# Kernel optimization log

Hardware: AMD Instinct MI355X
Metric: run time of the kernel (lower is better)

## Reference

```python
import jax, jax.numpy as jnp
import numpy as np

HEADS = 8
KS = 7
PAD = 3


def grouped_conv1x1(x, w):
    # x: (B, Cin, H, W), w: (heads, Cout/h, Cin/h) -> (B, Cout, H, W)
    B, Cin, H, W = x.shape
    g, co, ci = w.shape
    xg = x.reshape(B, g, ci, H, W)
    out = jnp.einsum('bgchw,goc->bgohw', xg, w)
    return out.reshape(B, g * co, H, W)


def unfold2d(p, k):
    # p: (B, C, Hp, Wp) -> (B, C, H, W, k, k) sliding windows, stride 1
    B, C, Hp, Wp = p.shape
    H, W = Hp - k + 1, Wp - k + 1
    rows = [jnp.stack([p[:, :, i:i + H, j:j + W] for j in range(k)], axis=-1)
            for i in range(k)]
    return jnp.stack(rows, axis=-2)  # (B,C,H,W,k,k)


def setup_inputs() -> dict:
    key = jax.random.key(0)
    ks = jax.random.split(key, 7)
    B, Cin, H, W = 8, 64, 64, 64
    Cout = 64
    g = HEADS
    return {
        'x': jax.random.normal(ks[0], (B, Cin, H, W), jnp.float32),
        'r': jax.random.normal(ks[1], (1,), jnp.float32),
        'w_q': jax.random.normal(ks[2], (g, Cout // g, Cin // g), jnp.float32) * 0.2,
        'w_k': jax.random.normal(ks[3], (g, Cout // g, Cin // g), jnp.float32) * 0.2,
        'w_v': jax.random.normal(ks[4], (g, Cout // g, Cin // g), jnp.float32) * 0.2,
        'rel_h': jax.random.normal(ks[5], (Cout // 2, KS), jnp.float32),
        'rel_w': jax.random.normal(ks[6], (Cout // 2, KS), jnp.float32),
    }


def reference(x, r, w_q, w_k, w_v, rel_h, rel_w):
    B, Cin, H, W = x.shape
    g = HEADS
    Cout = w_q.shape[0] * w_q.shape[1]
    dh = Cout // g

    padded = jnp.pad(x, ((0, 0), (0, 0), (PAD, PAD), (PAD, PAD)))
    q = grouped_conv1x1(x, w_q)            # (B, Cout, H, W)
    k = grouped_conv1x1(padded, w_k)       # (B, Cout, H+2p, W+2p)
    v = grouped_conv1x1(padded, w_v)

    k = unfold2d(k, KS)                    # (B, Cout, H, W, KS, KS)
    v = unfold2d(v, KS)

    # learnable relative positional encoding: split channels in half,
    # add rel_h along window-height, rel_w along window-width
    half = Cout // 2
    k_h = k[:, :half] + rel_h[None, :, None, None, :, None]
    k_w = k[:, half:] + rel_w[None, :, None, None, None, :]
    k = jnp.concatenate([k_h, k_w], axis=1)

    K2 = KS * KS
    k = k.reshape(B, g, dh, H, W, K2)
    v = v.reshape(B, g, dh, H, W, K2)
    q = q.reshape(B, g, dh, H, W, 1)

    scale = np.sqrt(g / Cout).astype(np.float32)
    logits = (q * k).sum(axis=2, keepdims=True) * scale   # (B,g,1,H,W,K2)
    attn = jax.nn.softmax(logits, axis=-1)
    out = (attn * v).sum(axis=-1)                          # (B,g,dh,H,W)
    return out.reshape(B, Cout, H, W)
```

## Files before the change

kernel.cpp:

```cpp
#include <hip/hip_runtime.h>
#include <math.h>

#define NG  8
#define DH  8
#define NCP 4
#define KS  7
#define PAD 3
#define TH  16
#define TW  32
#define OW  2
#define TPH 22
#define RSTW 40
#define PLW  (TPH * RSTW)
#define CH  64
#define HH  64
#define WW  64

typedef __fp16 h2v __attribute__((ext_vector_type(2)));
typedef __fp16 h4v __attribute__((ext_vector_type(4)));

#if __has_builtin(__builtin_amdgcn_exp2f)
#define EXP2(x) __builtin_amdgcn_exp2f(x)
#else
#define EXP2(x) exp2f(x)
#endif

__device__ __forceinline__ int imin(int a, int b) { return a < b ? a : b; }
__device__ __forceinline__ int imax(int a, int b) { return a > b ? a : b; }

__global__ __launch_bounds__(256, 2)
void saconv_kernel(const float* __restrict__ x,
                   const float* __restrict__ wq,
                   const float* __restrict__ wk,
                   const float* __restrict__ wv,
                   const float* __restrict__ relh,
                   const float* __restrict__ relw,
                   float* __restrict__ out) {
  __shared__ h2v xs2[NCP * PLW];
  __shared__ float swq[DH * DH];
  __shared__ float swk[DH * DH];
  __shared__ float swv[DH * DH];
  __shared__ float srel[DH * KS];

  const int tx  = threadIdx.x;
  const int ty  = threadIdx.y;
  const int tid = ty * 16 + tx;
  const int bz  = blockIdx.z;
  const int b   = bz >> 3;
  const int g   = bz & 7;
  const int h0  = blockIdx.y * TH;
  const int w0  = blockIdx.x * TW;

  if (tid < DH * DH) swq[tid] = wq[g * DH * DH + tid];
  else if (tid < 2 * DH * DH) swk[tid - 64] = wk[g * DH * DH + tid - 64];
  else if (tid < 3 * DH * DH) swv[tid - 128] = wv[g * DH * DH + tid - 128];
  else if (tid < 3 * DH * DH + DH * KS) {
    int t2 = tid - 192;
    int c = t2 / KS, t = t2 - c * KS;
    int gc = g * DH + c;
    srel[t2] = (g < 4) ? relh[gc * KS + t] : relw[(gc - 32) * KS + t];
  }

  const float* xb = x + (size_t)(b * CH + g * DH) * (HH * WW);
  const int NCHK = NCP * TPH * 19;
  #pragma unroll
  for (int kk = 0; kk < 7; kk++) {
    int f = tid + kk * 256;
    if (f < NCHK) {
      int cp  = f / (TPH * 19);
      int r   = f - cp * (TPH * 19);
      int row = r / 19;
      int cc  = r - row * 19;
      int yy  = h0 + row - PAD;
      int cy  = imin(imax(yy, 0), HH - 1);
      bool yok = (yy >= 0) & (yy < HH);
      const float* p0 = xb + ((size_t)(2 * cp) * HH + cy) * WW;
      float v0[2], v1[2];
      #pragma unroll
      for (int e = 0; e < 2; e++) {
        int xx = w0 + 2 * cc + e - PAD;
        int cx = imin(imax(xx, 0), WW - 1);
        bool inb = yok & (xx >= 0) & (xx < WW);
        float a0 = p0[cx];
        float a1 = p0[HH * WW + cx];
        v0[e] = inb ? a0 : 0.0f;
        v1[e] = inb ? a1 : 0.0f;
      }
      h2v pk0 = __builtin_amdgcn_cvt_pkrtz(v0[0], v1[0]);
      h2v pk1 = __builtin_amdgcn_cvt_pkrtz(v0[1], v1[1]);
      h4v w4 = { pk0.x, pk0.y, pk1.x, pk1.y };
      *(h4v*)&xs2[cp * PLW + row * RSTW + 2 * cc] = w4;
    }
  }
  __syncthreads();

  const float scale = 0.35355339059327373f;
  const float L2E   = 1.4426950408889634f;
  h2v  qkh[OW][NCP];
  float rq[OW][KS];
  {
    float xc[OW][DH];
    #pragma unroll
    for (int o = 0; o < OW; o++)
      #pragma unroll
      for (int cp = 0; cp < NCP; cp++) {
        h2v wv2 = xs2[cp * PLW + (ty + PAD) * RSTW + (2 * tx + o + PAD)];
        xc[o][2 * cp]     = (float)wv2.x;
        xc[o][2 * cp + 1] = (float)wv2.y;
      }
    float q_[OW][DH];
    #pragma unroll
    for (int o = 0; o < OW; o++)
      #pragma unroll
      for (int c = 0; c < DH; c++) {
        float a = 0.f;
        #pragma unroll
        for (int ci = 0; ci < DH; ci++)
          a = fmaf(swq[c * DH + ci], xc[o][ci], a);
        q_[o][c] = a;
      }
    #pragma unroll
    for (int o = 0; o < OW; o++)
      #pragma unroll
      for (int cp = 0; cp < NCP; cp++) {
        float a0 = 0.f, a1 = 0.f;
        #pragma unroll
        for (int c = 0; c < DH; c++) {
          a0 = fmaf(q_[o][c], swk[c * DH + 2 * cp], a0);
          a1 = fmaf(q_[o][c], swk[c * DH + 2 * cp + 1], a1);
        }
        qkh[o][cp] = __builtin_amdgcn_cvt_pkrtz(a0 * (scale * L2E), a1 * (scale * L2E));
      }
    #pragma unroll
    for (int o = 0; o < OW; o++)
      #pragma unroll
      for (int t = 0; t < KS; t++) {
        float a = 0.f;
        #pragma unroll
        for (int c = 0; c < DH; c++)
          a = fmaf(q_[o][c], srel[c * KS + t], a);
        rq[o][t] = a * (scale * L2E);
      }
  }

  const bool useI = (g < 4);

  float s[OW], xa[OW][DH];
  #pragma unroll
  for (int o = 0; o < OW; o++) {
    s[o] = 0.f;
    #pragma unroll
    for (int ci = 0; ci < DH; ci++) xa[o][ci] = 0.f;
  }

  #pragma unroll
  for (int i = 0; i < KS; i++) {
    const int wbase = (ty + i) * RSTW + 2 * tx;
    h2v xw[NCP][8];
    #pragma unroll
    for (int cp = 0; cp < NCP; cp++) {
      const h4v* bp = (const h4v*)&xs2[cp * PLW + wbase];
      h4v r0 = bp[0], r1 = bp[1], r2 = bp[2], r3 = bp[3];
      xw[cp][0] = __builtin_shufflevector(r0, r0, 0, 1);
      xw[cp][1] = __builtin_shufflevector(r0, r0, 2, 3);
      xw[cp][2] = __builtin_shufflevector(r1, r1, 0, 1);
      xw[cp][3] = __builtin_shufflevector(r1, r1, 2, 3);
      xw[cp][4] = __builtin_shufflevector(r2, r2, 0, 1);
      xw[cp][5] = __builtin_shufflevector(r2, r2, 2, 3);
      xw[cp][6] = __builtin_shufflevector(r3, r3, 0, 1);
      xw[cp][7] = __builtin_shufflevector(r3, r3, 2, 3);
    }

    #pragma unroll
    for (int o = 0; o < OW; o++) {
      float e[KS];
      float se = 0.f;
      #pragma unroll
      for (int j = 0; j < KS; j++) {
        float d = useI ? rq[o][i] : rq[o][j];
        #pragma unroll
        for (int cp = 0; cp < NCP; cp++)
          d = __builtin_amdgcn_fdot2(qkh[o][cp], xw[cp][o + j], d, false);
        e[j] = EXP2(d);
        se += e[j];
      }
      s[o] += se;
      #pragma unroll
      for (int cp = 0; cp < NCP; cp++) {
        float a0 = xa[o][2 * cp];
        float a1 = xa[o][2 * cp + 1];
        #pragma unroll
        for (int j = 0; j < KS; j++) {
          a0 = fmaf(e[j], (float)xw[cp][o + j].x, a0);
          a1 = fmaf(e[j], (float)xw[cp][o + j].y, a1);
        }
        xa[o][2 * cp]     = a0;
        xa[o][2 * cp + 1] = a1;
      }
    }
  }

  #pragma unroll
  for (int o = 0; o < OW; o++) {
    float inv = 1.0f / s[o];
    #pragma unroll
    for (int ci = 0; ci < DH; ci++) xa[o][ci] *= inv;
  }

  const int h = h0 + ty;
  const int wbase = w0 + 2 * tx;
  #pragma unroll
  for (int c = 0; c < DH; c++) {
    float2 v2;
    {
      float a0 = 0.f, a1 = 0.f;
      #pragma unroll
      for (int ci = 0; ci < DH; ci++) {
        a0 = fmaf(swv[c * DH + ci], xa[0][ci], a0);
        a1 = fmaf(swv[c * DH + ci], xa[1][ci], a1);
      }
      v2.x = a0; v2.y = a1;
    }
    *(float2*)(&out[((size_t)(b * CH + g * DH + c) * HH + h) * WW + wbase]) = v2;
  }
}

extern "C" void kernel_launch(void* const* d_in, const int* in_sizes, int n_in,
                              void* d_out, int out_size, void* d_ws, size_t ws_size,
                              hipStream_t stream) {
  const float* x    = (const float*)d_in[0];
  const float* wq   = (const float*)d_in[2];
  const float* wk   = (const float*)d_in[3];
  const float* wv   = (const float*)d_in[4];
  const float* relh = (const float*)d_in[5];
  const float* relw = (const float*)d_in[6];
  float* out = (float*)d_out;

  const int B = in_sizes[0] / (CH * HH * WW);
  dim3 grid(WW / TW, HH / TH, B * NG);
  dim3 block(16, 16, 1);
  saconv_kernel<<<grid, block, 0, stream>>>(x, wq, wk, wv, relh, relw, out);
}
```

Baseline: 17.59 us.

## Compute one output pixel per thread and split columns by parity across blocks

Each thread used to compute two adjacent output columns. It now computes one, and the grid is doubled along x so that even and odd columns go to separate blocks. The x tile is loaded with a one-column shift per parity so the existing aligned LDS reads still work. This lowers register pressure and doubles the number of threads, which should raise occupancy. The cost is a duplicated halo load into LDS per block and strided scalar stores in place of float2 stores.

```diff
diff --git a/kernel.cpp b/kernel.cpp
--- a/kernel.cpp
+++ b/kernel.cpp
@@ -8,7 +8,6 @@
 #define PAD 3
 #define TH  16
 #define TW  32
-#define OW  2
 #define TPH 22
 #define RSTW 40
 #define PLW  (TPH * RSTW)
@@ -45,11 +44,13 @@
   const int tx  = threadIdx.x;
   const int ty  = threadIdx.y;
   const int tid = ty * 16 + tx;
+  const int gx  = blockIdx.x;
+  const int par = gx & 1;
+  const int w0  = (gx >> 1) * TW;
   const int bz  = blockIdx.z;
   const int b   = bz >> 3;
   const int g   = bz & 7;
   const int h0  = blockIdx.y * TH;
-  const int w0  = blockIdx.x * TW;
 
   if (tid < DH * DH) swq[tid] = wq[g * DH * DH + tid];
   else if (tid < 2 * DH * DH) swk[tid - 64] = wk[g * DH * DH + tid - 64];
@@ -78,7 +79,7 @@
       float v0[2], v1[2];
       #pragma unroll
       for (int e = 0; e < 2; e++) {
-        int xx = w0 + 2 * cc + e - PAD;
+        int xx = w0 + par + 2 * cc + e - PAD;
         int cx = imin(imax(xx, 0), WW - 1);
         bool inb = yok & (xx >= 0) & (xx < WW);
         float a0 = p0[cx];
@@ -96,62 +97,51 @@
 
   const float scale = 0.35355339059327373f;
   const float L2E   = 1.4426950408889634f;
-  h2v  qkh[OW][NCP];
-  float rq[OW][KS];
+  h2v  qkh[NCP];
+  float rq[KS];
   {
-    float xc[OW][DH];
-    #pragma unroll
-    for (int o = 0; o < OW; o++)
-      #pragma unroll
-      for (int cp = 0; cp < NCP; cp++) {
-        h2v wv2 = xs2[cp * PLW + (ty + PAD) * RSTW + (2 * tx + o + PAD)];
-        xc[o][2 * cp]     = (float)wv2.x;
-        xc[o][2 * cp + 1] = (float)wv2.y;
+    float xc[DH];
+    #pragma unroll
+    for (int cp = 0; cp < NCP; cp++) {
+      h2v wv2 = xs2[cp * PLW + (ty + PAD) * RSTW + (2 * tx + PAD)];
+      xc[2 * cp]     = (float)wv2.x;
+      xc[2 * cp + 1] = (float)wv2.y;
+    }
+    float q_[DH];
+    #pragma unroll
+    for (int c = 0; c < DH; c++) {
+      float a = 0.f;
+      #pragma unroll
+      for (int ci = 0; ci < DH; ci++)
+        a = fmaf(swq[c * DH + ci], xc[ci], a);
+      q_[c] = a;
+    }
+    #pragma unroll
+    for (int cp = 0; cp < NCP; cp++) {
+      float a0 = 0.f, a1 = 0.f;
+      #pragma unroll
+      for (int c = 0; c < DH; c++) {
+        a0 = fmaf(q_[c], swk[c * DH + 2 * cp], a0);
+        a1 = fmaf(q_[c], swk[c * DH + 2 * cp + 1], a1);
       }
-    float q_[OW][DH];
-    #pragma unroll
-    for (int o = 0; o < OW; o++)
-      #pragma unroll
-      for (int c = 0; c < DH; c++) {
-        float a = 0.f;
-        #pragma unroll
-        for (int ci = 0; ci < DH; ci++)
-          a = fmaf(swq[c * DH + ci], xc[o][ci], a);
-        q_[o][c] = a;
-      }
-    #pragma unroll
-    for (int o = 0; o < OW; o++)
-      #pragma unroll
-      for (int cp = 0; cp < NCP; cp++) {
-        float a0 = 0.f, a1 = 0.f;
-        #pragma unroll
-        for (int c = 0; c < DH; c++) {
-          a0 = fmaf(q_[o][c], swk[c * DH + 2 * cp], a0);
-          a1 = fmaf(q_[o][c], swk[c * DH + 2 * cp + 1], a1);
-        }
-        qkh[o][cp] = __builtin_amdgcn_cvt_pkrtz(a0 * (scale * L2E), a1 * (scale * L2E));
-      }
-    #pragma unroll
-    for (int o = 0; o < OW; o++)
-      #pragma unroll
-      for (int t = 0; t < KS; t++) {
-        float a = 0.f;
-        #pragma unroll
-        for (int c = 0; c < DH; c++)
-          a = fmaf(q_[o][c], srel[c * KS + t], a);
-        rq[o][t] = a * (scale * L2E);
-      }
+      qkh[cp] = __builtin_amdgcn_cvt_pkrtz(a0 * (scale * L2E), a1 * (scale * L2E));
+    }
+    #pragma unroll
+    for (int t = 0; t < KS; t++) {
+      float a = 0.f;
+      #pragma unroll
+      for (int c = 0; c < DH; c++)
+        a = fmaf(q_[c], srel[c * KS + t], a);
+      rq[t] = a * (scale * L2E);
+    }
   }
 
   const bool useI = (g < 4);
 
-  float s[OW], xa[OW][DH];
-  #pragma unroll
-  for (int o = 0; o < OW; o++) {
-    s[o] = 0.f;
-    #pragma unroll
-    for (int ci = 0; ci < DH; ci++) xa[o][ci] = 0.f;
-  }
+  float s = 0.f;
+  float xa[DH];
+  #pragma unroll
+  for (int ci = 0; ci < DH; ci++) xa[ci] = 0.f;
 
   #pragma unroll
   for (int i = 0; i < KS; i++) {
@@ -171,57 +161,46 @@
       xw[cp][7] = __builtin_shufflevector(r3, r3, 2, 3);
     }
 
-    #pragma unroll
-    for (int o = 0; o < OW; o++) {
-      float e[KS];
-      float se = 0.f;
+    float e[KS];
+    float se = 0.f;
+    #pragma unroll
+    for (int j = 0; j < KS; j++) {
+      float d = useI ? rq[i] : rq[j];
+      #pragma unroll
+      for (int cp = 0; cp < NCP; cp++)
+        d = __builtin_amdgcn_fdot2(qkh[cp], xw[cp][j], d, false);
+      e[j] = EXP2(d);
+      se += e[j];
+    }
+    s += se;
+    #pragma unroll
+    for (int cp = 0; cp < NCP; cp++) {
+      float a0 = xa[2 * cp];
+      float a1 = xa[2 * cp + 1];
       #pragma unroll
       for (int j = 0; j < KS; j++) {
-        float d = useI ? rq[o][i] : rq[o][j];
-        #pragma unroll
-        for (int cp = 0; cp < NCP; cp++)
-          d = __builtin_amdgcn_fdot2(qkh[o][cp], xw[cp][o + j], d, false);
-        e[j] = EXP2(d);
-        se += e[j];
+        a0 = fmaf(e[j], (float)xw[cp][j].x, a0);
+        a1 = fmaf(e[j], (float)xw[cp][j].y, a1);
       }
-      s[o] += se;
-      #pragma unroll
-      for (int cp = 0; cp < NCP; cp++) {
-        float a0 = xa[o][2 * cp];
-        float a1 = xa[o][2 * cp + 1];
-        #pragma unroll
-        for (int j = 0; j < KS; j++) {
-          a0 = fmaf(e[j], (float)xw[cp][o + j].x, a0);
-          a1 = fmaf(e[j], (float)xw[cp][o + j].y, a1);
-        }
-        xa[o][2 * cp]     = a0;
-        xa[o][2 * cp + 1] = a1;
-      }
-    }
-  }
-
-  #pragma unroll
-  for (int o = 0; o < OW; o++) {
-    float inv = 1.0f / s[o];
-    #pragma unroll
-    for (int ci = 0; ci < DH; ci++) xa[o][ci] *= inv;
-  }
+      xa[2 * cp]     = a0;
+      xa[2 * cp + 1] = a1;
+    }
+  }
+
+  float inv = 1.0f / s;
+  #pragma unroll
+  for (int ci = 0; ci < DH; ci++) xa[ci] *= inv;
 
   const int h = h0 + ty;
-  const int wbase = w0 + 2 * tx;
+  const int wcol = w0 + 2 * tx + par;
+  float* ob = out + (((size_t)(b * CH + g * DH) * HH + h) * WW + wcol);
   #pragma unroll
   for (int c = 0; c < DH; c++) {
-    float2 v2;
-    {
-      float a0 = 0.f, a1 = 0.f;
-      #pragma unroll
-      for (int ci = 0; ci < DH; ci++) {
-        a0 = fmaf(swv[c * DH + ci], xa[0][ci], a0);
-        a1 = fmaf(swv[c * DH + ci], xa[1][ci], a1);
-      }
-      v2.x = a0; v2.y = a1;
-    }
-    *(float2*)(&out[((size_t)(b * CH + g * DH + c) * HH + h) * WW + wbase]) = v2;
+    float a = 0.f;
+    #pragma unroll
+    for (int ci = 0; ci < DH; ci++)
+      a = fmaf(swv[c * DH + ci], xa[ci], a);
+    ob[(size_t)c * (HH * WW)] = a;
   }
 }
 
@@ -237,7 +216,7 @@
   float* out = (float*)d_out;
 
   const int B = in_sizes[0] / (CH * HH * WW);
-  dim3 grid(WW / TW, HH / TH, B * NG);
+  dim3 grid((WW / TW) * 2, HH / TH, B * NG);
   dim3 block(16, 16, 1);
   saconv_kernel<<<grid, block, 0, stream>>>(x, wq, wk, wv, relh, relw, out);
 }
```

Result: slower. 26.11 us (+48.4%).

## Compute q projections from global x before barrier, drop shared weight staging

Applied to the files above, without the earlier changes.

Weights and relative encodings are now read directly from global memory, which is uniform per block and likely ends up in scalar loads, instead of being staged in shared memory. The query projection reads x from global in fp32 and runs before the barrier, so it overlaps with the shared-memory tile fill. The window loop is specialised per head half (g<4 vs not), removing the per-iteration select. The trade-off is extra global loads and code size in exchange for shorter barrier stalls and slightly higher precision on q.

```diff
diff --git a/kernel.cpp b/kernel.cpp
--- a/kernel.cpp
+++ b/kernel.cpp
@@ -37,10 +37,6 @@
                    const float* __restrict__ relw,
                    float* __restrict__ out) {
   __shared__ h2v xs2[NCP * PLW];
-  __shared__ float swq[DH * DH];
-  __shared__ float swk[DH * DH];
-  __shared__ float swv[DH * DH];
-  __shared__ float srel[DH * KS];
 
   const int tx  = threadIdx.x;
   const int ty  = threadIdx.y;
@@ -50,16 +46,6 @@
   const int g   = bz & 7;
   const int h0  = blockIdx.y * TH;
   const int w0  = blockIdx.x * TW;
-
-  if (tid < DH * DH) swq[tid] = wq[g * DH * DH + tid];
-  else if (tid < 2 * DH * DH) swk[tid - 64] = wk[g * DH * DH + tid - 64];
-  else if (tid < 3 * DH * DH) swv[tid - 128] = wv[g * DH * DH + tid - 128];
-  else if (tid < 3 * DH * DH + DH * KS) {
-    int t2 = tid - 192;
-    int c = t2 / KS, t = t2 - c * KS;
-    int gc = g * DH + c;
-    srel[t2] = (g < 4) ? relh[gc * KS + t] : relw[(gc - 32) * KS + t];
-  }
 
   const float* xb = x + (size_t)(b * CH + g * DH) * (HH * WW);
   const int NCHK = NCP * TPH * 19;
@@ -92,22 +78,19 @@
       *(h4v*)&xs2[cp * PLW + row * RSTW + 2 * cc] = w4;
     }
   }
-  __syncthreads();
-
-  const float scale = 0.35355339059327373f;
-  const float L2E   = 1.4426950408889634f;
+
+  const float sl2e = 0.35355339059327373f * 1.4426950408889634f;
   h2v  qkh[OW][NCP];
   float rq[OW][KS];
   {
     float xc[OW][DH];
+    const float* xq = xb + (size_t)(h0 + ty) * WW + (w0 + 2 * tx);
     #pragma unroll
     for (int o = 0; o < OW; o++)
       #pragma unroll
-      for (int cp = 0; cp < NCP; cp++) {
-        h2v wv2 = xs2[cp * PLW + (ty + PAD) * RSTW + (2 * tx + o + PAD)];
-        xc[o][2 * cp]     = (float)wv2.x;
-        xc[o][2 * cp + 1] = (float)wv2.y;
-      }
+      for (int ci = 0; ci < DH; ci++)
+        xc[o][ci] = xq[(size_t)ci * (HH * WW) + o];
+
     float q_[OW][DH];
     #pragma unroll
     for (int o = 0; o < OW; o++)
@@ -116,7 +99,7 @@
         float a = 0.f;
         #pragma unroll
         for (int ci = 0; ci < DH; ci++)
-          a = fmaf(swq[c * DH + ci], xc[o][ci], a);
+          a = fmaf(wq[(g * DH + c) * DH + ci], xc[o][ci], a);
         q_[o][c] = a;
       }
     #pragma unroll
@@ -126,24 +109,36 @@
         float a0 = 0.f, a1 = 0.f;
         #pragma unroll
         for (int c = 0; c < DH; c++) {
-          a0 = fmaf(q_[o][c], swk[c * DH + 2 * cp], a0);
-          a1 = fmaf(q_[o][c], swk[c * DH + 2 * cp + 1], a1);
+          a0 = fmaf(q_[o][c], wk[(g * DH + c) * DH + 2 * cp], a0);
+          a1 = fmaf(q_[o][c], wk[(g * DH + c) * DH + 2 * cp + 1], a1);
         }
-        qkh[o][cp] = __builtin_amdgcn_cvt_pkrtz(a0 * (scale * L2E), a1 * (scale * L2E));
+        qkh[o][cp] = __builtin_amdgcn_cvt_pkrtz(a0 * sl2e, a1 * sl2e);
       }
-    #pragma unroll
-    for (int o = 0; o < OW; o++)
-      #pragma unroll
-      for (int t = 0; t < KS; t++) {
-        float a = 0.f;
-        #pragma unroll
-        for (int c = 0; c < DH; c++)
-          a = fmaf(q_[o][c], srel[c * KS + t], a);
-        rq[o][t] = a * (scale * L2E);
-      }
-  }
-
-  const bool useI = (g < 4);
+    if (g < 4) {
+      #pragma unroll
+      for (int o = 0; o < OW; o++)
+        #pragma unroll
+        for (int t = 0; t < KS; t++) {
+          float a = 0.f;
+          #pragma unroll
+          for (int c = 0; c < DH; c++)
+            a = fmaf(q_[o][c], relh[(g * DH + c) * KS + t], a);
+          rq[o][t] = a * sl2e;
+        }
+    } else {
+      #pragma unroll
+      for (int o = 0; o < OW; o++)
+        #pragma unroll
+        for (int t = 0; t < KS; t++) {
+          float a = 0.f;
+          #pragma unroll
+          for (int c = 0; c < DH; c++)
+            a = fmaf(q_[o][c], relw[((g - 4) * DH + c) * KS + t], a);
+          rq[o][t] = a * sl2e;
+        }
+    }
+  }
+  __syncthreads();
 
   float s[OW], xa[OW][DH];
   #pragma unroll
@@ -153,52 +148,49 @@
     for (int ci = 0; ci < DH; ci++) xa[o][ci] = 0.f;
   }
 
-  #pragma unroll
-  for (int i = 0; i < KS; i++) {
-    const int wbase = (ty + i) * RSTW + 2 * tx;
-    h2v xw[NCP][8];
-    #pragma unroll
-    for (int cp = 0; cp < NCP; cp++) {
-      const h4v* bp = (const h4v*)&xs2[cp * PLW + wbase];
-      h4v r0 = bp[0], r1 = bp[1], r2 = bp[2], r3 = bp[3];
-      xw[cp][0] = __builtin_shufflevector(r0, r0, 0, 1);
-      xw[cp][1] = __builtin_shufflevector(r0, r0, 2, 3);
-      xw[cp][2] = __builtin_shufflevector(r1, r1, 0, 1);
-      xw[cp][3] = __builtin_shufflevector(r1, r1, 2, 3);
-      xw[cp][4] = __builtin_shufflevector(r2, r2, 0, 1);
-      xw[cp][5] = __builtin_shufflevector(r2, r2, 2, 3);
-      xw[cp][6] = __builtin_shufflevector(r3, r3, 0, 1);
-      xw[cp][7] = __builtin_shufflevector(r3, r3, 2, 3);
-    }
-
-    #pragma unroll
-    for (int o = 0; o < OW; o++) {
-      float e[KS];
-      float se = 0.f;
-      #pragma unroll
-      for (int j = 0; j < KS; j++) {
-        float d = useI ? rq[o][i] : rq[o][j];
-        #pragma unroll
-        for (int cp = 0; cp < NCP; cp++)
-          d = __builtin_amdgcn_fdot2(qkh[o][cp], xw[cp][o + j], d, false);
-        e[j] = EXP2(d);
-        se += e[j];
-      }
-      s[o] += se;
-      #pragma unroll
-      for (int cp = 0; cp < NCP; cp++) {
-        float a0 = xa[o][2 * cp];
-        float a1 = xa[o][2 * cp + 1];
-        #pragma unroll
-        for (int j = 0; j < KS; j++) {
-          a0 = fmaf(e[j], (float)xw[cp][o + j].x, a0);
-          a1 = fmaf(e[j], (float)xw[cp][o + j].y, a1);
-        }
-        xa[o][2 * cp]     = a0;
-        xa[o][2 * cp + 1] = a1;
-      }
-    }
-  }
+#define WINLOOP(DINIT)                                                         \
+  _Pragma("unroll")                                                            \
+  for (int i = 0; i < KS; i++) {                                               \
+    const int wbase = (ty + i) * RSTW + 2 * tx;                                \
+    h2v xw[NCP][8];                                                            \
+    _Pragma("unroll")                                                          \
+    for (int cp = 0; cp < NCP; cp++) {                                         \
+      const h2v* bp = &xs2[cp * PLW + wbase];                                  \
+      _Pragma("unroll")                                                        \
+      for (int k = 0; k < 8; k++) xw[cp][k] = bp[k];                           \
+    }                                                                          \
+    _Pragma("unroll")                                                          \
+    for (int o = 0; o < OW; o++) {                                             \
+      float e[KS];                                                             \
+      float se = 0.f;                                                          \
+      _Pragma("unroll")                                                        \
+      for (int j = 0; j < KS; j++) {                                           \
+        float d = (DINIT);                                                     \
+        _Pragma("unroll")                                                      \
+        for (int cp = 0; cp < NCP; cp++)                                       \
+          d = __builtin_amdgcn_fdot2(qkh[o][cp], xw[cp][o + j], d, false);     \
+        e[j] = EXP2(d);                                                        \
+        se += e[j];                                                            \
+      }                                                                        \
+      s[o] += se;                                                              \
+      _Pragma("unroll")                                                        \
+      for (int cp = 0; cp < NCP; cp++) {                                       \
+        float a0 = xa[o][2 * cp];                                              \
+        float a1 = xa[o][2 * cp + 1];                                          \
+        _Pragma("unroll")                                                      \
+        for (int j = 0; j < KS; j++) {                                         \
+          a0 = fmaf(e[j], (float)xw[cp][o + j].x, a0);                         \
+          a1 = fmaf(e[j], (float)xw[cp][o + j].y, a1);                         \
+        }                                                                      \
+        xa[o][2 * cp]     = a0;                                                \
+        xa[o][2 * cp + 1] = a1;                                                \
+      }                                                                        \
+    }                                                                          \
+  }
+
+  if (g < 4) { WINLOOP(rq[o][i]) }
+  else       { WINLOOP(rq[o][j]) }
+#undef WINLOOP
 
   #pragma unroll
   for (int o = 0; o < OW; o++) {
@@ -211,17 +203,15 @@
   const int wbase = w0 + 2 * tx;
   #pragma unroll
   for (int c = 0; c < DH; c++) {
-    float2 v2;
-    {
-      float a0 = 0.f, a1 = 0.f;
-      #pragma unroll
-      for (int ci = 0; ci < DH; ci++) {
-        a0 = fmaf(swv[c * DH + ci], xa[0][ci], a0);
-        a1 = fmaf(swv[c * DH + ci], xa[1][ci], a1);
-      }
-      v2.x = a0; v2.y = a1;
+    float a0 = 0.f, a1 = 0.f;
+    #pragma unroll
+    for (int ci = 0; ci < DH; ci++) {
+      float wvv = wv[(g * DH + c) * DH + ci];
+      a0 = fmaf(wvv, xa[0][ci], a0);
+      a1 = fmaf(wvv, xa[1][ci], a1);
     }
-    *(float2*)(&out[((size_t)(b * CH + g * DH + c) * HH + h) * WW + wbase]) = v2;
+    *(float2*)(&out[((size_t)(b * CH + g * DH + c) * HH + h) * WW + wbase]) =
+        make_float2(a0, a1);
   }
 }
 
```

Measured after the change: 18.57 us. 1.06x slower.
